# Optimization experiments

Measured on AMD Instinct MI355X. Metric: run time of the kernel, lower is better.

Reference implementation:

```python
import jax, jax.numpy as jnp
import numpy as np

B, S, T = 32, 512, 32
EMB, HID = 256, 512
VOCAB, OOV = 50000, 100


def setup_inputs() -> dict:
    key = jax.random.key(0)
    ks = jax.random.split(key, 20)
    g = lambda k, shape: (0.02 * jax.random.normal(k, shape)).astype(jnp.float32)
    return {
        "dec_input_ids": jax.random.randint(ks[0], (B, T), 0, VOCAB),
        "enc_ids_ext": jax.random.randint(ks[1], (B, S), 0, VOCAB + OOV),
        "encoder_states": jax.random.normal(ks[2], (B, S, HID), jnp.float32),
        "enc_padding_mask": jnp.ones((B, S), jnp.float32),
        "init_h": jax.random.normal(ks[3], (B, HID), jnp.float32),
        "init_c": jax.random.normal(ks[4], (B, HID), jnp.float32),
        "embeddings": g(ks[5], (VOCAB, EMB)),
        "W_enc": g(ks[6], (HID, HID)),
        "b_enc": jnp.zeros((HID,), jnp.float32),
        "W_attn": g(ks[7], (2 * HID, HID)),
        "v": g(ks[8], (HID,)),
        "w_cov": g(ks[9], (HID,)),
        "b_cov": jnp.zeros((HID,), jnp.float32),
        "W_x": g(ks[10], (EMB + HID, HID)),
        "W_out": g(ks[11], (2 * HID, HID)),
        "Wk": g(ks[12], (HID, 4 * HID)),
        "Wr": g(ks[13], (HID, 4 * HID)),
        "b_lstm": jnp.zeros((4 * HID,), jnp.float32),
        "W_pgen": g(ks[14], (4 * HID, 1)),
        "W_proj": g(ks[15], (HID, VOCAB)),
        "b_proj": jnp.zeros((VOCAB,), jnp.float32),
    }


def reference(dec_input_ids, enc_ids_ext, encoder_states, enc_padding_mask,
              init_h, init_c, embeddings, W_enc, b_enc, W_attn, v, w_cov,
              b_cov, W_x, W_out, Wk, Wr, b_lstm, W_pgen, W_proj, b_proj):
    Bq = encoder_states.shape[0]
    # 1x1 conv over [B,S,1,H] == pointwise linear
    enc_feat = jnp.einsum('bsh,hv->bsv', encoder_states, W_enc) + b_enc  # [B,S,V]
    emb = jnp.swapaxes(embeddings[dec_input_ids], 0, 1)  # [T,B,E]
    rows = jnp.arange(Bq)[:, None]

    def lstm(x, h, c):
        z = x @ Wk + h @ Wr + b_lstm
        i, f, g_, o = jnp.split(z, 4, axis=-1)
        c2 = jax.nn.sigmoid(f) * c + jax.nn.sigmoid(i) * jnp.tanh(g_)
        h2 = jax.nn.sigmoid(o) * jnp.tanh(c2)
        return h2, c2

    def attend(h, c, cov):
        dec_feat = jnp.concatenate([h, c], -1) @ W_attn  # [B,V]
        feats = enc_feat + dec_feat[:, None, :]
        if cov is not None:  # 1x1 conv on coverage [B,S,1,1] -> [B,S,V]
            feats = feats + cov[..., None] * w_cov + b_cov
        e = jnp.sum(v * jnp.tanh(feats), -1)  # [B,S]
        attn = jax.nn.softmax(e, axis=-1) * enc_padding_mask
        attn = attn / jnp.sum(attn, -1, keepdims=True)
        ctx = jnp.einsum('bs,bsv->bv', attn, enc_feat)
        return ctx, attn

    def decode(inp, h, c, ctx, cov):
        x = jnp.concatenate([inp, ctx], -1) @ W_x
        h, c = lstm(x, h, c)
        ctx, attn = attend(h, c, cov)
        p_gen = jax.nn.sigmoid(jnp.concatenate([ctx, h, c, x], -1) @ W_pgen)  # [B,1]
        out = jnp.concatenate([h, ctx], -1) @ W_out
        vocab_dist = jax.nn.softmax(out @ W_proj + b_proj, axis=-1)
        ext = jnp.concatenate([p_gen * vocab_dist,
                               jnp.zeros((Bq, OOV), vocab_dist.dtype)], -1)
        final = ext.at[rows, enc_ids_ext].add((1.0 - p_gen) * attn)
        return h, c, ctx, attn, p_gen, final

    # step 0: coverage starts as None, initialized from first attn dist
    ctx0 = jnp.zeros((Bq, HID), encoder_states.dtype)
    h, c, ctx, attn0, pg0, final0 = decode(emb[0], init_h, init_c, ctx0, None)
    cov = attn0

    def scan_step(carry, inp):
        h, c, ctx, cov = carry
        h, c, ctx, attn, pg, final = decode(inp, h, c, ctx, cov)
        return (h, c, ctx, cov + attn), final

    (_, _, _, cov), finals = jax.lax.scan(scan_step, (h, c, ctx, cov), emb[1:])
    final_dists = jnp.concatenate([final0[None], finals], axis=0)  # [T,B,VOCAB+OOV]
    return final_dists
```

## Files before the change

### kernel.cpp

```cpp
#include <hip/hip_runtime.h>
#include <math.h>

#define Bq 32
#define Sq 512
#define Tq 32
#define EMBq 256
#define HIDq 512
#define VOCABq 50000
#define OOVq 100
#define VEXTq (VOCABq + OOVq)
#define HALF_N 25088

typedef unsigned short u16;
typedef unsigned long long u64;
typedef __attribute__((ext_vector_type(8))) short bf16x8;
typedef __attribute__((ext_vector_type(4))) float f32x4;

__device__ __forceinline__ float sigmoidf_(float x){ return 1.0f/(1.0f+__expf(-x)); }
__device__ __forceinline__ float tanhf_(float x){ return 1.0f - 2.0f/(__expf(2.0f*x)+1.0f); }

__device__ __forceinline__ u16 f2bf(float x){
  union{float f; unsigned u;} v; v.f=x;
  unsigned r = v.u + 0x7FFFu + ((v.u>>16)&1u);
  return (u16)(r>>16);
}
__device__ __forceinline__ float bf2f(u16 h){
  union{unsigned u; float f;} v; v.u = ((unsigned)h)<<16; return v.f;
}

__device__ __forceinline__ float ld1(const float* p){
  return __hip_atomic_load((float*)p, __ATOMIC_RELAXED, __HIP_MEMORY_SCOPE_AGENT);
}
__device__ __forceinline__ void st1(float* p, float v){
  __hip_atomic_store(p, v, __ATOMIC_RELAXED, __HIP_MEMORY_SCOPE_AGENT);
}
__device__ __forceinline__ float2 ld2(const float* p){
  u64 v = __hip_atomic_load((u64*)p, __ATOMIC_RELAXED, __HIP_MEMORY_SCOPE_AGENT);
  union{u64 u; float2 f;} c; c.u=v; return c.f;
}
__device__ __forceinline__ void atadd(float* p, float v){
  __hip_atomic_fetch_add(p, v, __ATOMIC_RELAXED, __HIP_MEMORY_SCOPE_AGENT);
}

__device__ __forceinline__ void mbar(unsigned* gs, int sc, unsigned tag){
  asm volatile("s_waitcnt vmcnt(0)" ::: "memory");
  __syncthreads();
  if (threadIdx.x==0)
    __hip_atomic_store(gs+sc, tag, __ATOMIC_RELAXED, __HIP_MEMORY_SCOPE_AGENT);
  if (threadIdx.x<64){
    for(;;){
      unsigned v = (threadIdx.x<8)
        ? __hip_atomic_load(gs+threadIdx.x, __ATOMIC_RELAXED, __HIP_MEMORY_SCOPE_AGENT)
        : tag;
      if (__all(v>=tag)) break;
      __builtin_amdgcn_s_sleep(1);
    }
  }
  __syncthreads();
}

__device__ __forceinline__ float blockSum512(float v, float* red){
  #pragma unroll
  for (int off=32; off>0; off>>=1) v += __shfl_down(v, off);
  int lane = threadIdx.x & 63, wid = threadIdx.x >> 6;
  __syncthreads();
  if (lane==0) red[wid]=v;
  __syncthreads();
  float t=0.f;
  #pragma unroll
  for (int w=0;w<8;++w) t+=red[w];
  return t;
}

__global__ __launch_bounds__(256) void k_wet(const float* __restrict__ W, u16* __restrict__ WT){
  __shared__ float T[32][33];
  const int n0 = blockIdx.x*32, k0 = blockIdx.y*32;
  const int tid=threadIdx.x;
  #pragma unroll
  for (int it=0; it<4; ++it){
    int id = tid+it*256; int kk=id>>5, nn=id&31;
    T[kk][nn] = W[(size_t)(k0+kk)*512 + n0+nn];
  }
  __syncthreads();
  #pragma unroll
  for (int it=0; it<4; ++it){
    int id=tid+it*256; int nn=id>>5, kk=id&31;
    WT[(size_t)(n0+nn)*512 + k0+kk] = f2bf(T[kk][nn]);
  }
}

__global__ __launch_bounds__(256) void k_encm(const float* __restrict__ es,
    const u16* __restrict__ WET, const float* __restrict__ b_enc,
    u16* __restrict__ EFbf){
  __shared__ u16 As[128*40];
  __shared__ u16 Bs[128*40];
  const int tid=threadIdx.x;
  const int m0 = blockIdx.x*128, n0 = blockIdx.y*128;
  const int wid=tid>>6, lane=tid&63;
  const int wm=(wid>>1)*64, wn=(wid&1)*64;
  const int l15=lane&15, l4=lane>>4;
  f32x4 acc[4][4];
  #pragma unroll
  for (int mi=0;mi<4;++mi)
    #pragma unroll
    for (int ni=0;ni<4;++ni) acc[mi][ni] = (f32x4){0.f,0.f,0.f,0.f};
  for (int kt=0; kt<16; ++kt){
    const int k0=kt*32;
    __syncthreads();
    #pragma unroll
    for (int it=0; it<4; ++it){
      int id=tid+it*256; int row=id>>3, q=id&7;
      float4 v = *(const float4*)(es + (size_t)(m0+row)*512 + k0 + q*4);
      u64 pk = (u64)f2bf(v.x) | ((u64)f2bf(v.y)<<16) | ((u64)f2bf(v.z)<<32) | ((u64)f2bf(v.w)<<48);
      *(u64*)&As[row*40 + q*4] = pk;
    }
    #pragma unroll
    for (int it=0; it<2; ++it){
      int id=tid+it*256; int row=id>>2, c4=id&3;
      uint4 v = *(const uint4*)(WET + (size_t)(n0+row)*512 + k0 + c4*8);
      *(uint4*)&Bs[row*40 + c4*8] = v;
    }
    __syncthreads();
    bf16x8 a[4], b[4];
    #pragma unroll
    for (int mi=0;mi<4;++mi) a[mi] = *(const bf16x8*)(&As[(wm+mi*16+l15)*40 + l4*8]);
    #pragma unroll
    for (int ni=0;ni<4;++ni) b[ni] = *(const bf16x8*)(&Bs[(wn+ni*16+l15)*40 + l4*8]);
    #pragma unroll
    for (int mi=0;mi<4;++mi)
      #pragma unroll
      for (int ni=0;ni<4;++ni)
        acc[mi][ni] = __builtin_amdgcn_mfma_f32_16x16x32_bf16(a[mi], b[ni], acc[mi][ni], 0,0,0);
  }
  #pragma unroll
  for (int ni=0;ni<4;++ni){
    const int col = n0+wn+ni*16+l15;
    const float bp = b_enc[col];
    #pragma unroll
    for (int mi=0;mi<4;++mi){
      const int rb = m0+wm+mi*16+l4*4;
      #pragma unroll
      for (int r=0;r<4;++r)
        EFbf[(size_t)(rb+r)*512 + col] = f2bf(acc[mi][ni][r]+bp);
    }
  }
}

__global__ __launch_bounds__(512) void k_embx(const int* __restrict__ dec_ids,
  const float* __restrict__ emb, const float* __restrict__ W_x,
  const float* __restrict__ Wpgen, float* __restrict__ embx, float* __restrict__ embxp){
  __shared__ float A[16][257];
  __shared__ int ids[16];
  __shared__ float red[8];
  const int tid = threadIdx.x, r0 = blockIdx.x*16;
  if (tid<16){
    int row = r0+tid, tt = row>>5, bb = row&31;
    ids[tid] = dec_ids[bb*Tq + tt];
  }
  __syncthreads();
  for (int idx=tid; idx<16*256; idx+=512){
    int rr = idx>>8, kk = idx&255;
    A[rr][kk] = emb[(size_t)ids[rr]*EMBq + kk];
  }
  __syncthreads();
  float acc[16];
  #pragma unroll
  for (int r=0;r<16;++r) acc[r]=0.f;
  for (int k=0;k<256;++k){
    float w = W_x[(size_t)k*HIDq + tid];
    #pragma unroll
    for (int r=0;r<16;++r) acc[r] += A[r][k]*w;
  }
  float wp4 = Wpgen[1536+tid];
  for (int r=0;r<16;++r){
    embx[(size_t)(r0+r)*HIDq + tid] = acc[r];
    float s = blockSum512(acc[r]*wp4, red);
    if (tid==0) embxp[r0+r] = s;
  }
}

__global__ __launch_bounds__(512) void k_embz(const float* __restrict__ embx,
  const float* __restrict__ Wk, const float* __restrict__ b_lstm, float* __restrict__ embz){
  __shared__ float A[16][513];
  const int tid = threadIdx.x;
  const int r0 = blockIdx.x*16;
  const int n  = blockIdx.y*512 + tid;
  for (int idx=tid; idx<16*512; idx+=512){
    int rr=idx>>9, kk=idx&511;
    A[rr][kk] = embx[(size_t)(r0+rr)*HIDq + kk];
  }
  __syncthreads();
  float acc[16];
  #pragma unroll
  for (int r=0;r<16;++r) acc[r]=0.f;
  for (int k=0;k<512;++k){
    float w = Wk[(size_t)k*2048 + n];
    #pragma unroll
    for (int r=0;r<16;++r) acc[r] += A[r][k]*w;
  }
  float bl = b_lstm[n];
  #pragma unroll
  for (int r=0;r<16;++r) embz[(size_t)(r0+r)*2048 + n] = acc[r]+bl;
}

__global__ __launch_bounds__(512) void k_wxk(const float* __restrict__ Wk,
    const float* __restrict__ W_x, float* __restrict__ WXKT_){
  __shared__ float KT[32][64];
  __shared__ float X2[32][33];
  const int tid = threadIdx.x;
  const int n0 = blockIdx.x * 64;
  const int j0 = blockIdx.y * 32;
  const int jj = tid & 31;
  const int ng = tid >> 5;
  float acc[4] = {0,0,0,0};
  for (int i0=0;i0<512;i0+=32){
    __syncthreads();
    for (int idx=tid; idx<32*64; idx+=512){
      int ii = idx>>6, nn = idx&63;
      KT[ii][nn] = Wk[(size_t)(i0+ii)*2048 + n0+nn];
    }
    for (int idx=tid; idx<32*32; idx+=512){
      int j2 = idx>>5, i2 = idx&31;
      X2[j2][i2] = W_x[(size_t)(256+j0+j2)*HIDq + i0+i2];
    }
    __syncthreads();
    for (int ii=0;ii<32;++ii){
      float xv = X2[jj][ii];
      #pragma unroll
      for (int q=0;q<4;++q) acc[q] += KT[ii][ng*4+q]*xv;
    }
  }
  #pragma unroll
  for (int q=0;q<4;++q) WXKT_[(size_t)(n0+ng*4+q)*512 + j0+jj] = acc[q];
}

__global__ __launch_bounds__(512) void k_trans(const float* __restrict__ in,
    float* __restrict__ out, int K, int N){
  __shared__ float T[32][33];
  const int n0 = blockIdx.x*32, k0 = blockIdx.y*32;
  const int tid = threadIdx.x;
  for (int idx=tid; idx<1024; idx+=512){
    int kk = idx>>5, nn = idx&31;
    T[kk][nn] = in[(size_t)(k0+kk)*N + n0+nn];
  }
  __syncthreads();
  for (int idx=tid; idx<1024; idx+=512){
    int nn = idx>>5, kk = idx&31;
    out[(size_t)(n0+nn)*K + k0+kk] = T[kk][nn];
  }
}

__global__ __launch_bounds__(512) void k_wgc(const float* __restrict__ WXKT_,
    const float* __restrict__ WrT_, u16* __restrict__ WGC){
  const int np = blockIdx.x;
  const int colg = np>>2, g = np&3;
  const int n = g*512 + colg;
  const int sc = np>>8, npl = np&255;
  u16* o = WGC + (size_t)sc*262144 + (size_t)npl*8;
  const int k = threadIdx.x;
  float v0 = WXKT_[(size_t)n*512 + k];
  float v1 = WrT_[(size_t)n*512 + k];
  o[(size_t)(k>>3)*2048 + (k&7)] = f2bf(v0);
  const int k2 = k + 512;
  o[(size_t)(k2>>3)*2048 + (k2&7)] = f2bf(v1);
}

__global__ void k_cvt(const float* __restrict__ in, u16* __restrict__ out, int n){
  int i = blockIdx.x*256 + threadIdx.x;
  if (i<n) out[i] = f2bf(in[i]);
}

__global__ __launch_bounds__(512) void k_wp(const float* __restrict__ W_x,
  const float* __restrict__ Wpgen, float* __restrict__ Wxp){
  int j = threadIdx.x;
  const float* row = W_x + (size_t)(256+j)*HIDq;
  float s=0.f;
  for (int i=0;i<512;++i) s += row[i]*Wpgen[1536+i];
  Wxp[j] = s;
}

__global__ __launch_bounds__(1024,1) void k_rec8(
  const u16* __restrict__ EFbf, const float* __restrict__ mask,
  const float* __restrict__ init_h, const float* __restrict__ init_c,
  const u16* __restrict__ WGC, const float* __restrict__ embz,
  const u16* __restrict__ WAbf, const float* __restrict__ vvec,
  const float* __restrict__ wcov, const float* __restrict__ bcov,
  const float* __restrict__ Wpgen, const float* __restrict__ Wxp,
  float* __restrict__ Hg, float* __restrict__ ctx_acc,
  float* __restrict__ df_acc, float* __restrict__ Z_acc,
  float* __restrict__ hc_ws, float* __restrict__ attn_ws,
  float* __restrict__ pgen_raw, unsigned* __restrict__ msl)
{
  __shared__ float xA[1024];
  __shared__ float zl4[4][256];
  __shared__ float zfin[256];
  __shared__ float hsl[64], csl[64];
  __shared__ float covb[64], wsv[64], coldv[64];
  __shared__ float dfp[1024];
  __shared__ float dfl[512];
  __shared__ float ctp[1024];
  __shared__ float el[64];
  __shared__ float Zsh;

  const int tid = threadIdx.x, bid = blockIdx.x;
  const int lane = tid&63, wv = tid>>6;
  const int sc = bid & 7, bB = bid >> 3, s0 = sc*64;
  const int j0l = lane*8;
  unsigned* gs = msl + bB*16;

  float vvr[8], wcr[8], bcr[8];
  *(float4*)&vvr[0] = *(const float4*)&vvec[j0l]; *(float4*)&vvr[4] = *(const float4*)&vvec[j0l+4];
  *(float4*)&wcr[0] = *(const float4*)&wcov[j0l]; *(float4*)&wcr[4] = *(const float4*)&wcov[j0l+4];
  *(float4*)&bcr[0] = *(const float4*)&bcov[j0l]; *(float4*)&bcr[4] = *(const float4*)&bcov[j0l+4];

  if (tid<64) csl[tid] = init_c[bB*512 + s0 + tid];

  const int colL = tid & 255;
  const int kq = tid >> 8;
  const u16* wbase = WGC + (size_t)sc*262144 + (size_t)(kq*32)*2048 + (size_t)colL*8;
  const float* xs = &xA[kq*256];

  unsigned mt = 0;

  for (int t=0; t<Tq; ++t){
    if (t==0){
      if (tid<1024){
        if (tid<512) xA[tid] = 0.f;
        else xA[tid] = init_h[bB*512 + (tid-512)];
      }
      if (tid<64) st1(ctx_acc + bB*512 + s0+tid, 0.f);
      if (tid==0 && sc==0) st1(Z_acc + bB, 0.f);
      __syncthreads();
    } else {
      const int pr = (t-1)&1;
      float2 cf, hf; float Zl = 0.f;
      if (tid<256) cf = ld2(ctx_acc + (size_t)pr*16384 + bB*512 + tid*2);
      else if (tid<512) hf = ld2(Hg + (size_t)pr*16384 + bB*512 + (tid-256)*2);
      if (tid==0)  Zl = ld1(Z_acc + pr*32 + bB);
      if (tid<64)  coldv[tid] = xA[s0+tid];
      if (tid==0)  Zsh = Zl;
      __syncthreads();
      const float Z = Zsh;
      if (tid<256){ xA[tid*2] = cf.x/Z; xA[tid*2+1] = cf.y/Z; }
      else if (tid<512){ xA[512+(tid-256)*2] = hf.x; xA[512+(tid-256)*2+1] = hf.y; }
      __syncthreads();
      if (tid<64){
        const int j = s0+tid;
        float cxj = xA[j];
        __builtin_nontemporal_store(cxj, hc_ws + ((size_t)(t-1)*Bq+bB)*1024 + 512 + j);
        float a = wsv[tid]/Z;
        __builtin_nontemporal_store(a, attn_ws + ((size_t)(t-1)*Bq+bB)*Sq + j);
        covb[tid] = (t==1) ? a : covb[tid]+a;
        float part = cxj*Wpgen[j] + hsl[tid]*Wpgen[512+j]
                   + csl[tid]*Wpgen[1024+j] + coldv[tid]*Wxp[j];
        #pragma unroll
        for (int off=32; off>0; off>>=1) part += __shfl_down(part, off);
        if (tid==0) atadd(pgen_raw + (t-1)*Bq + bB, part);
      }
      if (tid<64) st1(ctx_acc + (size_t)(t&1)*16384 + bB*512 + s0+tid, 0.f);
      if (tid==0 && sc==0) st1(Z_acc + (t&1)*32 + bB, 0.f);
      __syncthreads();
    }
    {
      float acc = 0.f;
      #pragma unroll 8
      for (int kb=0; kb<32; ++kb){
        bf16x8 w8 = *(const bf16x8*)(wbase + (size_t)kb*2048);
        const u16* ph = (const u16*)&w8;
        float4 x0 = *(const float4*)(xs + kb*8);
        float4 x1 = *(const float4*)(xs + kb*8 + 4);
        acc += x0.x*bf2f(ph[0]) + x0.y*bf2f(ph[1]) + x0.z*bf2f(ph[2]) + x0.w*bf2f(ph[3])
             + x1.x*bf2f(ph[4]) + x1.y*bf2f(ph[5]) + x1.z*bf2f(ph[6]) + x1.w*bf2f(ph[7]);
      }
      zl4[kq][colL] = acc;
    }
    __syncthreads();
    if (tid<256) zfin[tid] = (zl4[0][tid]+zl4[1][tid]) + (zl4[2][tid]+zl4[3][tid]);
    __syncthreads();
    if (tid<64){
      const int colg = s0 + tid;
      const float* ez = embz + ((size_t)t*Bq + bB)*2048 + colg;
      float zi = zfin[tid*4+0] + __builtin_nontemporal_load(ez);
      float zf = zfin[tid*4+1] + __builtin_nontemporal_load(ez+512);
      float zg = zfin[tid*4+2] + __builtin_nontemporal_load(ez+1024);
      float zo = zfin[tid*4+3] + __builtin_nontemporal_load(ez+1536);
      float co = csl[tid];
      float cn = sigmoidf_(zf)*co + sigmoidf_(zi)*tanhf_(zg);
      float hn = sigmoidf_(zo)*tanhf_(cn);
      csl[tid] = cn;
      hsl[tid] = hn;
      st1(Hg + (size_t)(t&1)*16384 + bB*512 + colg, hn);
      __builtin_nontemporal_store(hn, hc_ws + ((size_t)t*Bq+bB)*1024 + colg);
    }
    __syncthreads();
    {
      const int j = tid & 511, half = tid >> 9;
      const float* st = half ? csl : hsl;
      const u16* wa = WAbf + (size_t)(half*512 + s0)*512 + j;
      float acc = 0.f;
      #pragma unroll 8
      for (int k=0;k<64;++k) acc += st[k]*bf2f(wa[(size_t)k*512]);
      dfp[tid] = acc;
    }
    __syncthreads();
    if (tid<512) atadd(df_acc + (size_t)(t&1)*16384 + bB*512 + tid, dfp[tid]+dfp[512+tid]);
    ++mt; mbar(gs, sc, mt);
    if (tid<256){
      float2 f = ld2(df_acc + (size_t)(t&1)*16384 + bB*512 + tid*2);
      dfl[tid*2]=f.x; dfl[tid*2+1]=f.y;
    } else if (tid>=960){
      st1(df_acc + (size_t)((t+1)&1)*16384 + bB*512 + s0 + (tid-960), 0.f);
    }
    __syncthreads();
    {
      float dd[8];
      *(float4*)&dd[0] = *(const float4*)&dfl[j0l];
      *(float4*)&dd[4] = *(const float4*)&dfl[j0l+4];
      const u16* efb = EFbf + ((size_t)(bB*512 + s0))*512;
      #pragma unroll
      for (int r=0;r<4;++r){
        int sl = wv*4 + r;
        uint4 pack = *(const uint4*)(efb + (size_t)sl*512 + j0l);
        const u16* ph = (const u16*)&pack;
        float a8 = 0.f;
        if (t>0){
          float cvs = covb[sl];
          #pragma unroll
          for (int q=0;q<8;++q) a8 += vvr[q]*tanhf_(bf2f(ph[q])+dd[q]+cvs*wcr[q]+bcr[q]);
        } else {
          #pragma unroll
          for (int q=0;q<8;++q) a8 += vvr[q]*tanhf_(bf2f(ph[q])+dd[q]);
        }
        #pragma unroll
        for (int off=32; off>0; off>>=1) a8 += __shfl_down(a8, off);
        if (lane==0) el[sl] = a8;
      }
    }
    __syncthreads();
    if (tid<64){
      float w_ = mask[bB*512+s0+tid]*__expf(el[tid]);
      wsv[tid] = w_;
      float Zc = w_;
      #pragma unroll
      for (int off=32; off>0; off>>=1) Zc += __shfl_xor(Zc, off);
      if (tid==0) atadd(Z_acc + (t&1)*32 + bB, Zc);
    }
    __syncthreads();
    {
      const int j = tid & 511, sh = tid >> 9;
      const u16* efc = EFbf + ((size_t)(bB*512 + s0 + sh*32))*512 + j;
      float acc = 0.f;
      #pragma unroll 4
      for (int s=0;s<32;++s) acc += wsv[sh*32+s]*bf2f(efc[(size_t)s*512]);
      ctp[tid] = acc;
    }
    __syncthreads();
    if (tid<512) atadd(ctx_acc + (size_t)(t&1)*16384 + bB*512 + tid, ctp[tid]+ctp[512+tid]);
    ++mt; mbar(gs, sc, mt);
  }
  {
    const int pr = (Tq-1)&1;
    float2 cf; float Zl = 0.f;
    if (tid<256) cf = ld2(ctx_acc + (size_t)pr*16384 + bB*512 + tid*2);
    if (tid==0)  Zl = ld1(Z_acc + pr*32 + bB);
    if (tid<64)  coldv[tid] = xA[s0+tid];
    if (tid==0)  Zsh = Zl;
    __syncthreads();
    const float Z = Zsh;
    if (tid<256){ xA[tid*2] = cf.x/Z; xA[tid*2+1] = cf.y/Z; }
    __syncthreads();
    if (tid<64){
      const int j = s0+tid;
      float cxj = xA[j];
      __builtin_nontemporal_store(cxj, hc_ws + ((size_t)(Tq-1)*Bq+bB)*1024 + 512 + j);
      float a = wsv[tid]/Z;
      __builtin_nontemporal_store(a, attn_ws + ((size_t)(Tq-1)*Bq+bB)*Sq + j);
      float part = cxj*Wpgen[j] + hsl[tid]*Wpgen[512+j]
                 + csl[tid]*Wpgen[1024+j] + coldv[tid]*Wxp[j];
      #pragma unroll
      for (int off=32; off>0; off>>=1) part += __shfl_down(part, off);
      if (tid==0) atadd(pgen_raw + (Tq-1)*Bq + bB, part);
    }
  }
}

__global__ __launch_bounds__(512) void k_mid(const float* __restrict__ hc,
    const float* __restrict__ W_out, u16* __restrict__ outm_bf){
  __shared__ float A[16][256];
  const int tid=threadIdx.x;
  const int r0=blockIdx.x*16;
  float acc[16];
  #pragma unroll
  for (int r=0;r<16;++r) acc[r]=0.f;
  for (int kc=0;kc<4;++kc){
    __syncthreads();
    for (int i=tid;i<16*256;i+=512){
      int rr=i>>8, kk=i&255;
      A[rr][kk]=hc[(size_t)(r0+rr)*1024 + kc*256+kk];
    }
    __syncthreads();
    for (int k=0;k<256;++k){
      float w=W_out[(size_t)(kc*256+k)*HIDq + tid];
      #pragma unroll
      for (int r=0;r<16;++r) acc[r]+=A[r][k]*w;
    }
  }
  #pragma unroll
  for (int r=0;r<16;++r) outm_bf[(size_t)(r0+r)*HIDq+tid]=f2bf(acc[r]);
}

__global__ __launch_bounds__(256) void k_wcvt(const float* __restrict__ Wp,
    u16* __restrict__ WT, int n_base){
  __shared__ float T[32][33];
  const int n0 = blockIdx.x*32, k0 = blockIdx.y*32;
  const int tid = threadIdx.x;
  #pragma unroll
  for (int it=0; it<4; ++it){
    int id = tid + it*256;
    int kk = id>>5, nn = id&31;
    int gn = n_base + n0 + nn;
    T[kk][nn] = (gn < VOCABq) ? Wp[(size_t)(k0+kk)*VOCABq + gn] : 0.f;
  }
  __syncthreads();
  #pragma unroll
  for (int it=0; it<4; ++it){
    int id = tid + it*256;
    int nn = id>>5, kk = id&31;
    WT[(size_t)(n0+nn)*512 + k0+kk] = f2bf(T[kk][nn]);
  }
}

__global__ __launch_bounds__(256) void k_projs(const u16* __restrict__ Abf,
    const u16* __restrict__ WT, const float* __restrict__ b_proj,
    float* __restrict__ out, float* __restrict__ rowsum, int n_base){
  __shared__ u16 As[128*40];
  __shared__ u16 Bs[128*40];
  const int tid = threadIdx.x;
  const int m0 = blockIdx.x * 128;
  const int n0 = blockIdx.y * 128;
  const int wid = tid>>6, lane = tid&63;
  const int wm = (wid>>1)*64, wn = (wid&1)*64;
  const int l15 = lane&15, l4 = lane>>4;
  f32x4 acc[4][4];
  #pragma unroll
  for (int mi=0;mi<4;++mi)
    #pragma unroll
    for (int ni=0;ni<4;++ni) acc[mi][ni] = (f32x4){0.f,0.f,0.f,0.f};

  for (int kt=0; kt<16; ++kt){
    const int k0 = kt*32;
    __syncthreads();
    #pragma unroll
    for (int it=0; it<2; ++it){
      int id = tid + it*256;
      int row = id>>2, c4 = id&3;
      uint4 va = *(const uint4*)(Abf + (size_t)(m0+row)*512 + k0 + c4*8);
      *(uint4*)(&As[row*40 + c4*8]) = va;
      uint4 vb = *(const uint4*)(WT + (size_t)(n0+row)*512 + k0 + c4*8);
      *(uint4*)(&Bs[row*40 + c4*8]) = vb;
    }
    __syncthreads();
    bf16x8 a[4], b[4];
    #pragma unroll
    for (int mi=0;mi<4;++mi)
      a[mi] = *(const bf16x8*)(&As[(wm + mi*16 + l15)*40 + l4*8]);
    #pragma unroll
    for (int ni=0;ni<4;++ni)
      b[ni] = *(const bf16x8*)(&Bs[(wn + ni*16 + l15)*40 + l4*8]);
    #pragma unroll
    for (int mi=0;mi<4;++mi)
      #pragma unroll
      for (int ni=0;ni<4;++ni)
        acc[mi][ni] = __builtin_amdgcn_mfma_f32_16x16x32_bf16(a[mi], b[ni], acc[mi][ni], 0,0,0);
  }

  float prow[4][4];
  #pragma unroll
  for (int mi=0;mi<4;++mi)
    #pragma unroll
    for (int r=0;r<4;++r) prow[mi][r]=0.f;

  #pragma unroll
  for (int ni=0;ni<4;++ni){
    const int col = n_base + n0 + wn + ni*16 + l15;
    const bool ok = (col < VOCABq);
    const float bp = ok ? b_proj[col] : 0.f;
    #pragma unroll
    for (int mi=0;mi<4;++mi){
      const int rbase = m0 + wm + mi*16 + l4*4;
      #pragma unroll
      for (int r=0;r<4;++r){
        float p = ok ? __expf(acc[mi][ni][r] + bp) : 0.f;
        if (ok) out[(size_t)(rbase+r)*VEXTq + col] = p;
        prow[mi][r] += p;
      }
    }
  }
  #pragma unroll
  for (int mi=0;mi<4;++mi)
    #pragma unroll
    for (int r=0;r<4;++r){
      float v = prow[mi][r];
      v += __shfl_xor(v,1); v += __shfl_xor(v,2);
      v += __shfl_xor(v,4); v += __shfl_xor(v,8);
      if (l15==0) atadd(rowsum + m0 + wm + mi*16 + l4*4 + r, v);
    }
}

__global__ __launch_bounds__(256) void k_sm2(float* __restrict__ out,
    const float* __restrict__ rowsum, const float* __restrict__ pgen_raw,
    const float* __restrict__ embxp, const float* __restrict__ attn_ws,
    const int* __restrict__ enc_ids){
  const int row=blockIdx.x, tid=threadIdx.x;
  const int b = row & (Bq-1);
  float* orow = out + (size_t)row*VEXTq;
  const float pg = sigmoidf_(pgen_raw[row] + embxp[row]);
  const float scale = pg / rowsum[row];
  for (int i=tid;i<VOCABq;i+=256) orow[i] *= scale;
  for (int i=VOCABq+tid;i<VEXTq;i+=256) orow[i] = 0.f;
  __syncthreads();
  const float w1 = 1.f-pg;
  const float* arow = attn_ws + (size_t)row*Sq;
  const int* ids = enc_ids + b*Sq;
  for (int si=tid; si<Sq; si+=256)
    atomicAdd(&orow[ids[si]], w1*arow[si]);
}

extern "C" void kernel_launch(void* const* d_in, const int* in_sizes, int n_in,
                              void* d_out, int out_size, void* d_ws, size_t ws_size,
                              hipStream_t stream) {
  (void)in_sizes; (void)n_in; (void)out_size; (void)ws_size;
  const int*   dec_ids    = (const int*)  d_in[0];
  const int*   enc_ids    = (const int*)  d_in[1];
  const float* enc_states = (const float*)d_in[2];
  const float* mask       = (const float*)d_in[3];
  const float* init_h     = (const float*)d_in[4];
  const float* init_c     = (const float*)d_in[5];
  const float* embeddings = (const float*)d_in[6];
  const float* W_enc      = (const float*)d_in[7];
  const float* b_enc      = (const float*)d_in[8];
  const float* W_attn     = (const float*)d_in[9];
  const float* vvec       = (const float*)d_in[10];
  const float* w_cov      = (const float*)d_in[11];
  const float* b_cov      = (const float*)d_in[12];
  const float* W_x        = (const float*)d_in[13];
  const float* W_out      = (const float*)d_in[14];
  const float* Wk         = (const float*)d_in[15];
  const float* Wr         = (const float*)d_in[16];
  const float* b_lstm     = (const float*)d_in[17];
  const float* W_pgen     = (const float*)d_in[18];
  const float* W_proj     = (const float*)d_in[19];
  const float* b_proj     = (const float*)d_in[20];
  float* out = (float*)d_out;
  float* ws  = (float*)d_ws;

  u16*   EFbf    = (u16*)ws;
  float* attn_ws = ws + 4194304;
  float* hc_ws   = attn_ws + 524288;
  u16*   outm_bf = (u16*)(hc_ws + 1048576);
  float* embx    = hc_ws + 1048576 + 262144;
  float* embxp   = embx + 524288;
  float* embz    = embxp + 1024;
  float* WXKT_   = embz + 2097152;
  float* WrT_    = WXKT_ + 1048576;
  float* Wxp     = WrT_ + 1048576;
  float* Hg      = Wxp + 512;
  unsigned* msl  = (unsigned*)(Hg + 32768);
  float* pgen_raw= (float*)(msl + 512);
  float* ctx_acc = pgen_raw + 1024;
  float* df_acc  = ctx_acc + 32768;
  float* Z_acc   = df_acc + 32768;
  float* rowsum  = Z_acc + 64;
  u16*   WGC     = (u16*)(rowsum + 1024);
  u16*   WAbf    = (u16*)(((float*)WGC) + 1048576);
  u16*   WET     = (u16*)(((float*)WAbf) + 262144);
  u16*   WT      = (u16*)(((float*)WET) + 131072);

  hipMemsetAsync(msl, 0, (512 + 1024 + 32768 + 32768 + 64 + 1024)*sizeof(unsigned), stream);

  {
    dim3 g(16,16);
    k_wet<<<g, 256, 0, stream>>>(W_enc, WET);
  }
  {
    dim3 g(128,4);
    k_encm<<<g, 256, 0, stream>>>(enc_states, WET, b_enc, EFbf);
  }
  k_embx<<<64, 512, 0, stream>>>(dec_ids, embeddings, W_x, W_pgen, embx, embxp);
  {
    dim3 g(64,4);
    k_embz<<<g, 512, 0, stream>>>(embx, Wk, b_lstm, embz);
  }
  {
    dim3 g(32,16);
    k_wxk<<<g, 512, 0, stream>>>(Wk, W_x, WXKT_);
  }
  {
    dim3 g(64,16);
    k_trans<<<g, 512, 0, stream>>>(Wr, WrT_, 512, 2048);
  }
  k_wgc<<<2048, 512, 0, stream>>>(WXKT_, WrT_, WGC);
  k_cvt<<<(524288+255)/256, 256, 0, stream>>>(W_attn, WAbf, 524288);
  k_wp<<<1, 512, 0, stream>>>(W_x, W_pgen, Wxp);

  {
    void* args[] = { (void*)&EFbf, (void*)&mask, (void*)&init_h, (void*)&init_c,
                     (void*)&WGC, (void*)&embz, (void*)&WAbf, (void*)&vvec,
                     (void*)&w_cov, (void*)&b_cov, (void*)&W_pgen, (void*)&Wxp,
                     (void*)&Hg, (void*)&ctx_acc, (void*)&df_acc, (void*)&Z_acc,
                     (void*)&hc_ws, (void*)&attn_ws, (void*)&pgen_raw,
                     (void*)&msl };
    hipLaunchCooperativeKernel((void*)k_rec8, dim3(256), dim3(1024), args, 0, stream);
  }

  k_mid<<<(Tq*Bq)/16, 512, 0, stream>>>(hc_ws, W_out, outm_bf);
  for (int half=0; half<2; ++half){
    const int n_base = half*HALF_N;
    dim3 gc(HALF_N/32, 16);
    k_wcvt<<<gc, 256, 0, stream>>>(W_proj, WT, n_base);
    dim3 gp(8, HALF_N/128);
    k_projs<<<gp, 256, 0, stream>>>(outm_bf, WT, b_proj, out, rowsum, n_base);
  }
  k_sm2<<<Tq*Bq, 256, 0, stream>>>(out, rowsum, pgen_raw, embxp, attn_ws, enc_ids);
}
```

Before: 1.738 ms.

## Replace scalar fp32 precompute GEMMs with bf16 MFMA GEMM kernel

Replaces the scalar fp32 kernels that compute emb@Wk (embz) and the fused W_x·Wk product with a shared bf16 MFMA tiled GEMM. Wk is transposed to bf16 and W_x is converted to bf16 alongside a parallel pgen reduction that replaces a single-block loop. The final output scaling loop is also vectorised to float4. This adds bf16 rounding to precomputed weights and activations, which may affect accuracy.

New measurement: 1.584 ms. -8.8%, faster.

```diff
diff --git a/kernel.cpp b/kernel.cpp
--- a/kernel.cpp
+++ b/kernel.cpp
@@ -86,6 +86,87 @@
   for (int it=0; it<4; ++it){
     int id=tid+it*256; int nn=id>>5, kk=id&31;
     WT[(size_t)(n0+nn)*512 + k0+kk] = f2bf(T[kk][nn]);
+  }
+}
+
+__global__ __launch_bounds__(256) void k_wkt(const float* __restrict__ Wk, u16* __restrict__ WkT){
+  __shared__ float T[32][33];
+  const int n0 = blockIdx.x*32, k0 = blockIdx.y*32;
+  const int tid=threadIdx.x;
+  #pragma unroll
+  for (int it=0; it<4; ++it){
+    int id=tid+it*256; int kk=id>>5, nn=id&31;
+    T[kk][nn] = Wk[(size_t)(k0+kk)*2048 + n0+nn];
+  }
+  __syncthreads();
+  #pragma unroll
+  for (int it=0; it<4; ++it){
+    int id=tid+it*256; int nn=id>>5, kk=id&31;
+    WkT[(size_t)(n0+nn)*512 + k0+kk] = f2bf(T[kk][nn]);
+  }
+}
+
+__global__ __launch_bounds__(512) void k_wx2c(const float* __restrict__ W_x,
+    const float* __restrict__ Wpgen, u16* __restrict__ Xb, float* __restrict__ Wxp){
+  __shared__ float red[8];
+  const int j = blockIdx.x, i = threadIdx.x;
+  float v = W_x[(size_t)(256+j)*512 + i];
+  Xb[(size_t)j*512 + i] = f2bf(v);
+  float s = blockSum512(v*Wpgen[1536+i], red);
+  if (i==0) Wxp[j] = s;
+}
+
+__global__ __launch_bounds__(256) void k_gemm512(const u16* __restrict__ A,
+    const u16* __restrict__ B, const float* __restrict__ bias,
+    float* __restrict__ out, int ncols, int use_bias){
+  __shared__ u16 As[128*40];
+  __shared__ u16 Bs[128*40];
+  const int tid = threadIdx.x;
+  const int m0 = blockIdx.x * 128;
+  const int n0 = blockIdx.y * 128;
+  const int wid = tid>>6, lane = tid&63;
+  const int wm = (wid>>1)*64, wn = (wid&1)*64;
+  const int l15 = lane&15, l4 = lane>>4;
+  f32x4 acc[4][4];
+  #pragma unroll
+  for (int mi=0;mi<4;++mi)
+    #pragma unroll
+    for (int ni=0;ni<4;++ni) acc[mi][ni] = (f32x4){0.f,0.f,0.f,0.f};
+  for (int kt=0; kt<16; ++kt){
+    const int k0 = kt*32;
+    __syncthreads();
+    #pragma unroll
+    for (int it=0; it<2; ++it){
+      int id = tid + it*256;
+      int row = id>>2, c4 = id&3;
+      uint4 va = *(const uint4*)(A + (size_t)(m0+row)*512 + k0 + c4*8);
+      *(uint4*)(&As[row*40 + c4*8]) = va;
+      uint4 vb = *(const uint4*)(B + (size_t)(n0+row)*512 + k0 + c4*8);
+      *(uint4*)(&Bs[row*40 + c4*8]) = vb;
+    }
+    __syncthreads();
+    bf16x8 a[4], b[4];
+    #pragma unroll
+    for (int mi=0;mi<4;++mi) a[mi] = *(const bf16x8*)(&As[(wm+mi*16+l15)*40 + l4*8]);
+    #pragma unroll
+    for (int ni=0;ni<4;++ni) b[ni] = *(const bf16x8*)(&Bs[(wn+ni*16+l15)*40 + l4*8]);
+    #pragma unroll
+    for (int mi=0;mi<4;++mi)
+      #pragma unroll
+      for (int ni=0;ni<4;++ni)
+        acc[mi][ni] = __builtin_amdgcn_mfma_f32_16x16x32_bf16(a[mi], b[ni], acc[mi][ni], 0,0,0);
+  }
+  #pragma unroll
+  for (int ni=0;ni<4;++ni){
+    const int col = n0 + wn + ni*16 + l15;
+    const float bp = use_bias ? bias[col] : 0.f;
+    #pragma unroll
+    for (int mi=0;mi<4;++mi){
+      const int rbase = m0 + wm + mi*16 + l4*4;
+      #pragma unroll
+      for (int r=0;r<4;++r)
+        out[(size_t)(rbase+r)*ncols + col] = acc[mi][ni][r] + bp;
+    }
   }
 }
 
@@ -148,7 +229,7 @@
 
 __global__ __launch_bounds__(512) void k_embx(const int* __restrict__ dec_ids,
   const float* __restrict__ emb, const float* __restrict__ W_x,
-  const float* __restrict__ Wpgen, float* __restrict__ embx, float* __restrict__ embxp){
+  const float* __restrict__ Wpgen, u16* __restrict__ embx_bf, float* __restrict__ embxp){
   __shared__ float A[16][257];
   __shared__ int ids[16];
   __shared__ float red[8];
@@ -173,65 +254,10 @@
   }
   float wp4 = Wpgen[1536+tid];
   for (int r=0;r<16;++r){
-    embx[(size_t)(r0+r)*HIDq + tid] = acc[r];
+    embx_bf[(size_t)(r0+r)*HIDq + tid] = f2bf(acc[r]);
     float s = blockSum512(acc[r]*wp4, red);
     if (tid==0) embxp[r0+r] = s;
   }
-}
-
-__global__ __launch_bounds__(512) void k_embz(const float* __restrict__ embx,
-  const float* __restrict__ Wk, const float* __restrict__ b_lstm, float* __restrict__ embz){
-  __shared__ float A[16][513];
-  const int tid = threadIdx.x;
-  const int r0 = blockIdx.x*16;
-  const int n  = blockIdx.y*512 + tid;
-  for (int idx=tid; idx<16*512; idx+=512){
-    int rr=idx>>9, kk=idx&511;
-    A[rr][kk] = embx[(size_t)(r0+rr)*HIDq + kk];
-  }
-  __syncthreads();
-  float acc[16];
-  #pragma unroll
-  for (int r=0;r<16;++r) acc[r]=0.f;
-  for (int k=0;k<512;++k){
-    float w = Wk[(size_t)k*2048 + n];
-    #pragma unroll
-    for (int r=0;r<16;++r) acc[r] += A[r][k]*w;
-  }
-  float bl = b_lstm[n];
-  #pragma unroll
-  for (int r=0;r<16;++r) embz[(size_t)(r0+r)*2048 + n] = acc[r]+bl;
-}
-
-__global__ __launch_bounds__(512) void k_wxk(const float* __restrict__ Wk,
-    const float* __restrict__ W_x, float* __restrict__ WXKT_){
-  __shared__ float KT[32][64];
-  __shared__ float X2[32][33];
-  const int tid = threadIdx.x;
-  const int n0 = blockIdx.x * 64;
-  const int j0 = blockIdx.y * 32;
-  const int jj = tid & 31;
-  const int ng = tid >> 5;
-  float acc[4] = {0,0,0,0};
-  for (int i0=0;i0<512;i0+=32){
-    __syncthreads();
-    for (int idx=tid; idx<32*64; idx+=512){
-      int ii = idx>>6, nn = idx&63;
-      KT[ii][nn] = Wk[(size_t)(i0+ii)*2048 + n0+nn];
-    }
-    for (int idx=tid; idx<32*32; idx+=512){
-      int j2 = idx>>5, i2 = idx&31;
-      X2[j2][i2] = W_x[(size_t)(256+j0+j2)*HIDq + i0+i2];
-    }
-    __syncthreads();
-    for (int ii=0;ii<32;++ii){
-      float xv = X2[jj][ii];
-      #pragma unroll
-      for (int q=0;q<4;++q) acc[q] += KT[ii][ng*4+q]*xv;
-    }
-  }
-  #pragma unroll
-  for (int q=0;q<4;++q) WXKT_[(size_t)(n0+ng*4+q)*512 + j0+jj] = acc[q];
 }
 
 __global__ __launch_bounds__(512) void k_trans(const float* __restrict__ in,
@@ -268,15 +294,6 @@
 __global__ void k_cvt(const float* __restrict__ in, u16* __restrict__ out, int n){
   int i = blockIdx.x*256 + threadIdx.x;
   if (i<n) out[i] = f2bf(in[i]);
-}
-
-__global__ __launch_bounds__(512) void k_wp(const float* __restrict__ W_x,
-  const float* __restrict__ Wpgen, float* __restrict__ Wxp){
-  int j = threadIdx.x;
-  const float* row = W_x + (size_t)(256+j)*HIDq;
-  float s=0.f;
-  for (int i=0;i<512;++i) s += row[i]*Wpgen[1536+i];
-  Wxp[j] = s;
 }
 
 __global__ __launch_bounds__(1024,1) void k_rec8(
@@ -324,10 +341,8 @@
 
   for (int t=0; t<Tq; ++t){
     if (t==0){
-      if (tid<1024){
-        if (tid<512) xA[tid] = 0.f;
-        else xA[tid] = init_h[bB*512 + (tid-512)];
-      }
+      if (tid<512) xA[tid] = 0.f;
+      else xA[tid] = init_h[bB*512 + (tid-512)];
       if (tid<64) st1(ctx_acc + bB*512 + s0+tid, 0.f);
       if (tid==0 && sc==0) st1(Z_acc + bB, 0.f);
       __syncthreads();
@@ -616,7 +631,12 @@
   float* orow = out + (size_t)row*VEXTq;
   const float pg = sigmoidf_(pgen_raw[row] + embxp[row]);
   const float scale = pg / rowsum[row];
-  for (int i=tid;i<VOCABq;i+=256) orow[i] *= scale;
+  float4* o4 = (float4*)orow;
+  for (int i=tid;i<VOCABq/4;i+=256){
+    float4 v = o4[i];
+    v.x*=scale; v.y*=scale; v.z*=scale; v.w*=scale;
+    o4[i] = v;
+  }
   for (int i=VOCABq+tid;i<VEXTq;i+=256) orow[i] = 0.f;
   __syncthreads();
   const float w1 = 1.f-pg;
@@ -658,12 +678,14 @@
   float* attn_ws = ws + 4194304;
   float* hc_ws   = attn_ws + 524288;
   u16*   outm_bf = (u16*)(hc_ws + 1048576);
-  float* embx    = hc_ws + 1048576 + 262144;
-  float* embxp   = embx + 524288;
+  u16*   embx_bf = (u16*)(hc_ws + 1048576 + 262144);
+  float* embxp   = hc_ws + 1048576 + 262144 + 262144;
   float* embz    = embxp + 1024;
   float* WXKT_   = embz + 2097152;
   float* WrT_    = WXKT_ + 1048576;
-  float* Wxp     = WrT_ + 1048576;
+  u16*   WkT     = (u16*)(WrT_ + 1048576);
+  u16*   Xb      = (u16*)(((float*)WkT) + 524288);
+  float* Wxp     = ((float*)Xb) + 131072;
   float* Hg      = Wxp + 512;
   unsigned* msl  = (unsigned*)(Hg + 32768);
   float* pgen_raw= (float*)(msl + 512);
@@ -686,14 +708,19 @@
     dim3 g(128,4);
     k_encm<<<g, 256, 0, stream>>>(enc_states, WET, b_enc, EFbf);
   }
-  k_embx<<<64, 512, 0, stream>>>(dec_ids, embeddings, W_x, W_pgen, embx, embxp);
+  k_embx<<<64, 512, 0, stream>>>(dec_ids, embeddings, W_x, W_pgen, embx_bf, embxp);
   {
-    dim3 g(64,4);
-    k_embz<<<g, 512, 0, stream>>>(embx, Wk, b_lstm, embz);
-  }
+    dim3 g(64,16);
+    k_wkt<<<g, 256, 0, stream>>>(Wk, WkT);
+  }
+  k_wx2c<<<512, 512, 0, stream>>>(W_x, W_pgen, Xb, Wxp);
   {
-    dim3 g(32,16);
-    k_wxk<<<g, 512, 0, stream>>>(Wk, W_x, WXKT_);
+    dim3 g(8,16);
+    k_gemm512<<<g, 256, 0, stream>>>(embx_bf, WkT, b_lstm, embz, 2048, 1);
+  }
+  {
+    dim3 g(16,4);
+    k_gemm512<<<g, 256, 0, stream>>>(WkT, Xb, (const float*)0, WXKT_, 512, 0);
   }
   {
     dim3 g(64,16);
@@ -701,7 +728,6 @@
   }
   k_wgc<<<2048, 512, 0, stream>>>(WXKT_, WrT_, WGC);
   k_cvt<<<(524288+255)/256, 256, 0, stream>>>(W_attn, WAbf, 524288);
-  k_wp<<<1, 512, 0, stream>>>(W_x, W_pgen, Wxp);
 
   {
     void* args[] = { (void*)&EFbf, (void*)&mask, (void*)&init_h, (void*)&init_c,
```
